# Optimization experiments

Measured on AMD Instinct MI355X. Metric: run time of the kernel, lower is better.

The kernel has to match this reference:

```python
import jax, jax.numpy as jnp
import numpy as np


def _l2norm(x, axis=1, eps=1e-12):
    n = jnp.sqrt(jnp.sum(x * x, axis=axis, keepdims=True))
    return x / jnp.maximum(n, eps)


def _update(query, keys, labels, class_counts, num_classes):
    # Vectorized form of Memory.update + get_update_query (train branch).
    m, d = keys.shape
    q = _l2norm(query, axis=1)                              # [N, d]
    score = q @ keys.T                                      # [N, m]
    s_q = jax.nn.softmax(score, axis=0)                     # softmax over queries
    s_m = jax.nn.softmax(score, axis=1)                     # softmax over memory slots
    gather = jnp.argmax(s_m, axis=1)                        # top-1 slot per query, [N]
    # per-slot scatter-reduce: sum_{i: argmax_i==j} s_q[i,j]/max_i s_q[i,j] * q[i]
    w = s_q / jnp.max(s_q, axis=0, keepdims=True)           # [N, m]
    onehot = (gather[:, None] == jnp.arange(m)[None, :]).astype(q.dtype)
    qu = (w * onehot).T @ q                                 # [m, d]
    part = m // num_classes
    slot_class = jnp.arange(m) // part                      # class id of each slot
    active = (slot_class[:, None] == labels[None, :]).any(axis=1)
    qu = jnp.where(active[:, None], qu, 0.0)                # only slots of present classes
    # count-weighted running-average update; torch loop overwrites
    # updated_keys_final each iteration, so only the LAST unique label
    # (torch.unique is sorted -> max) takes effect. Faithful to that.
    last = jnp.max(labels)
    count = jnp.sum(labels == last).astype(q.dtype)
    in_part = slot_class == last
    temp = jnp.where(in_part, class_counts[last], 1.0)[:, None]   # [m, 1]
    updated = temp * keys + qu
    temp2 = temp + jnp.where(in_part, count, 0.0)[:, None]
    return _l2norm(updated / temp2, axis=1)                 # [m, d]


def _read(embedding, mem, num_classes):
    # Memory.read: per-partition block_compare, score is detached in torch.
    m, d = mem.shape
    pr = m // (num_classes - 1)
    nblk = m // pr
    qr = embedding.reshape(d, -1).T                         # [Nq, d]
    blocks = mem.reshape(nblk, pr, d)

    def blk(b):
        s = jax.lax.stop_gradient(b @ qr.T)                 # [pr, Nq] (detached)
        return s.T @ b                                      # [Nq, d]

    return jax.vmap(blk)(blocks)                            # [nblk, Nq, d]


def setup_inputs():
    key = jax.random.key(0)
    k1, k2, k3, k4, k5 = jax.random.split(key, 5)
    N, d, m, C, Nq, L = 8192, 256, 4608, 9, 16384, 16
    return {
        "query": jax.random.normal(k1, (N, d), jnp.float32),
        "embeddings_src": jax.random.normal(k2, (d, Nq), jnp.float32),
        "embeddings_tgt": jax.random.normal(k3, (d, Nq), jnp.float32),
        "keys": _l2norm(jax.random.normal(k4, (m, d), jnp.float32), axis=1),
        "class_counts": jnp.ones((C,), jnp.float32),
        "labels": jax.random.randint(k5, (L,), 1, C).astype(jnp.int32),
        "num_classes": C,
    }


def reference(query, embeddings_src, embeddings_tgt, keys, class_counts, labels, num_classes):
    mem = _update(query, keys, labels, class_counts, num_classes)
    feat_src = _read(embeddings_src, mem, num_classes)
    feat_tgt = _read(embeddings_tgt, mem, num_classes)
    return jnp.stack([feat_src, feat_tgt])                  # [2, nblk, Nq, d]
```

## Files before the change

kernel.cpp:

```cpp
#include <hip/hip_runtime.h>
#include <math.h>

#define NQRY 8192
#define DIM  256
#define MS   4608
#define NQE  16384
#define NBLK 8
#define PRROWS 576

typedef __attribute__((ext_vector_type(8))) short bf16x8;
typedef __attribute__((ext_vector_type(4))) float f32x4;
typedef __attribute__((ext_vector_type(16))) float f32x16;


__device__ __forceinline__ unsigned ordf(float f) {
  unsigned u = __float_as_uint(f);
  return (u & 0x80000000u) ? ~u : (u | 0x80000000u);
}
__device__ __forceinline__ float unordf(unsigned u) {
  unsigned b = (u & 0x80000000u) ? (u & 0x7FFFFFFFu) : ~u;
  return __uint_as_float(b);
}
__device__ __forceinline__ unsigned short bf16rn(float x) {
  unsigned u = __float_as_uint(x);
  unsigned r = u + 0x7FFFu + ((u >> 16) & 1u);
  return (unsigned short)(r >> 16);
}
__device__ __forceinline__ void splitbf(float x, unsigned short& h, unsigned short& lo) {
  unsigned u = __float_as_uint(x);
  h = (unsigned short)(u >> 16);
  float hf = __uint_as_float(u & 0xFFFF0000u);
  lo = bf16rn(x - hf);
}

#define PREP_NBLK 18070
#define ZERO_N4   300160
__global__ __launch_bounds__(256) void k_prep(
    const float* __restrict__ query, float* __restrict__ q,
    unsigned short* __restrict__ qh, unsigned short* __restrict__ ql,
    const float* __restrict__ keys,
    unsigned short* __restrict__ kh, unsigned short* __restrict__ kl,
    const float* __restrict__ embS, const float* __restrict__ embT,
    unsigned short* __restrict__ ebT,
    float4* __restrict__ zp,
    const int* __restrict__ labels, const float* __restrict__ cc,
    float* __restrict__ sc) {
  __shared__ float tile[64][33];
  int b = blockIdx.x, t = threadIdx.x;
  if (b < 8192) {
    size_t idx = (size_t)b * DIM + t;
    float x = query[idx];
    float v = x * x;
    #pragma unroll
    for (int o = 32; o; o >>= 1) v += __shfl_down(v, o);
    float* s = &tile[0][0];
    if ((t & 63) == 0) s[t >> 6] = v;
    __syncthreads();
    float ss = (s[0] + s[1]) + (s[2] + s[3]);
    float qq = x / fmaxf(sqrtf(ss), 1e-12f);
    q[idx] = qq;
    unsigned short h, lo;
    splitbf(qq, h, lo);
    qh[idx] = h; ql[idx] = lo;
  } else if (b < 12800) {
    size_t idx = (size_t)(b - 8192) * 256 + t;
    unsigned short h, lo;
    splitbf(keys[idx], h, lo);
    kh[idx] = h; kl[idx] = lo;
  } else if (b < 16896) {
    int bb = b - 12800;
    int x = bb & 511, y = (bb >> 9) & 3, z = bb >> 11;
    const float* emb = z ? embT : embS;
    int n0 = x * 32, k0 = y * 64;
    int kl2 = t >> 5, nl = t & 31;
    #pragma unroll
    for (int i = 0; i < 8; i++)
      tile[kl2 * 8 + i][nl] = emb[(size_t)(k0 + kl2 * 8 + i) * NQE + n0 + nl];
    __syncthreads();
    int nl2 = t >> 3, kq = (t & 7) * 8;
    bf16x8 hv;
    #pragma unroll
    for (int j = 0; j < 8; j++) hv[j] = (short)bf16rn(tile[kq + j][nl2]);
    *(bf16x8*)(ebT + (size_t)z * NQE * DIM + (size_t)(n0 + nl2) * DIM + k0 + kq) = hv;
  } else if (b < 18069) {
    int i = (b - 16896) * 256 + t;
    if (i < ZERO_N4) zp[i] = float4{0.f, 0.f, 0.f, 0.f};
  } else {
    if (t < 64) {
      int l = (t < 16) ? labels[t] : (int)0x80000000;
      int mx = l;
      #pragma unroll
      for (int o = 32; o; o >>= 1) mx = max(mx, __shfl_down(mx, o));
      mx = __shfl(mx, 0);
      int cnt = (t < 16 && l == mx) ? 1 : 0;
      #pragma unroll
      for (int o = 32; o; o >>= 1) cnt += __shfl_down(cnt, o);
      unsigned amv = (t < 16) ? (1u << l) : 0u;
      #pragma unroll
      for (int o = 32; o; o >>= 1) amv |= __shfl_down(amv, o);
      if (t == 0) {
        sc[0] = __int_as_float(mx);
        sc[1] = (float)cnt;
        sc[2] = cc[mx];
        sc[3] = __uint_as_float(amv);
      }
    }
  }
}

__global__ __launch_bounds__(256) void k_scoremax(
    const unsigned short* __restrict__ qh, const unsigned short* __restrict__ ql,
    const unsigned short* __restrict__ kh, const unsigned short* __restrict__ kl,
    unsigned long long* __restrict__ rowbest, unsigned* __restrict__ colmax) {
  __shared__ __align__(16) char smem[32768];
  char* sA = smem;
  char* sB = smem + 16384;
  int tid = threadIdx.x;
  int n0 = blockIdx.x * 128, m0 = blockIdx.y * 128;
  int w = tid >> 6, lane = tid & 63;
  int wm = w >> 1, wn = w & 1;
  int l31 = lane & 31, hi5 = lane >> 5;
  int srow = tid >> 3, sc8 = tid & 7;
  f32x16 acc[2][2] = {};
  for (int kk = 0; kk < 8; kk++) {
    __syncthreads();
    #pragma unroll
    for (int t = 0; t < 8; t++) {
      int row = (t & 3) * 32 + srow;
      const unsigned short* hsrc = (t < 4) ? qh : kh;
      const unsigned short* lsrc = (t < 4) ? ql : kl;
      int base = (t < 4) ? m0 : n0;
      const unsigned short* src =
          ((sc8 < 4) ? hsrc : lsrc) + (size_t)(base + row) * DIM + kk * 32 + (sc8 & 3) * 8;
      char* dst = ((t < 4) ? sA : sB) + row * 128 + ((sc8 ^ (row & 7)) << 4);
      *(bf16x8*)dst = *(const bf16x8*)src;
    }
    __syncthreads();
    bf16x8 ah[2][2], al[2][2];
    #pragma unroll
    for (int fm = 0; fm < 2; fm++) {
      int ra = wm * 64 + fm * 32 + l31;
      #pragma unroll
      for (int h = 0; h < 2; h++) {
        int ch = h * 2 + hi5;
        ah[fm][h] = *(const bf16x8*)(sA + ra * 128 + ((ch ^ (ra & 7)) << 4));
        al[fm][h] = *(const bf16x8*)(sA + ra * 128 + (((ch + 4) ^ (ra & 7)) << 4));
      }
    }
    #pragma unroll
    for (int fn = 0; fn < 2; fn++) {
      int rb = wn * 64 + fn * 32 + l31;
      bf16x8 bh[2], bl[2];
      #pragma unroll
      for (int h = 0; h < 2; h++) {
        int ch = h * 2 + hi5;
        bh[h] = *(const bf16x8*)(sB + rb * 128 + ((ch ^ (rb & 7)) << 4));
        bl[h] = *(const bf16x8*)(sB + rb * 128 + (((ch + 4) ^ (rb & 7)) << 4));
      }
      #pragma unroll
      for (int fm = 0; fm < 2; fm++)
        #pragma unroll
        for (int h = 0; h < 2; h++) {
          acc[fm][fn] = __builtin_amdgcn_mfma_f32_32x32x16_bf16(ah[fm][h], bh[h], acc[fm][fn], 0, 0, 0);
          acc[fm][fn] = __builtin_amdgcn_mfma_f32_32x32x16_bf16(ah[fm][h], bl[h], acc[fm][fn], 0, 0, 0);
          acc[fm][fn] = __builtin_amdgcn_mfma_f32_32x32x16_bf16(al[fm][h], bh[h], acc[fm][fn], 0, 0, 0);
        }
    }
  }
  #pragma unroll
  for (int fm = 0; fm < 2; fm++) {
    #pragma unroll
    for (int reg = 0; reg < 16; reg++) {
      unsigned long long p = 0ull;
      #pragma unroll
      for (int fn = 0; fn < 2; fn++) {
        float v = acc[fm][fn][reg];
        unsigned ng = (unsigned)(n0 + wn * 64 + fn * 32 + l31);
        unsigned long long cand =
            ((unsigned long long)ordf(v) << 32) | (unsigned long long)(0xFFFFFFFFu - ng);
        if (cand > p) p = cand;
      }
      #pragma unroll
      for (int o = 1; o < 32; o <<= 1) {
        unsigned long long t2 = __shfl_xor(p, o);
        if (t2 > p) p = t2;
      }
      if (l31 == 0) {
        int rl = (reg & 3) + 8 * (reg >> 2) + 4 * hi5;
        atomicMax(rowbest + (m0 + wm * 64 + fm * 32 + rl), p);
      }
    }
  }
  #pragma unroll
  for (int fn = 0; fn < 2; fn++) {
    float v = -3.4e38f;
    #pragma unroll
    for (int fm = 0; fm < 2; fm++)
      #pragma unroll
      for (int reg = 0; reg < 16; reg++) v = fmaxf(v, acc[fm][fn][reg]);
    v = fmaxf(v, __shfl_xor(v, 32));
    if (hi5 == 0) atomicMax(colmax + (n0 + wn * 64 + fn * 32 + l31), ordf(v));
  }
}

__global__ __launch_bounds__(256) void k_rowscatter(
    const unsigned long long* __restrict__ rowbest, const unsigned* __restrict__ colmax,
    const float* __restrict__ q, float* __restrict__ qu) {
  int i = blockIdx.x, t = threadIdx.x;
  unsigned long long p = rowbest[i];
  int g = (int)(0xFFFFFFFFu - (unsigned)(p & 0xFFFFFFFFull));
  float sv = unordf((unsigned)(p >> 32));
  float w = expf(sv - unordf(colmax[g]));
  atomicAdd(qu + (size_t)g * DIM + t, w * q[(size_t)i * DIM + t]);
}

__global__ __launch_bounds__(256) void k_mem(const float* __restrict__ keys,
                                             const float* __restrict__ qu,
                                             const float* __restrict__ sc,
                                             float* __restrict__ memr) {
  int j = blockIdx.x, t = threadIdx.x;
  int last = __float_as_int(sc[0]);
  float count = sc[1], ccl = sc[2];
  unsigned am = __float_as_uint(sc[3]);
  int cls = j >> 9;
  bool inp = (cls == last);
  float temp = inp ? ccl : 1.0f;
  float quv = ((am >> cls) & 1u) ? qu[(size_t)j * DIM + t] : 0.0f;
  float u = temp * keys[(size_t)j * DIM + t] + quv;
  float temp2 = temp + (inp ? count : 0.0f);
  float v = u / temp2;
  float vv = v * v;
  #pragma unroll
  for (int o = 32; o; o >>= 1) vv += __shfl_down(vv, o);
  __shared__ float s[4];
  if ((t & 63) == 0) s[t >> 6] = vv;
  __syncthreads();
  float ss = (s[0] + s[1]) + (s[2] + s[3]);
  memr[(size_t)j * DIM + t] = v / fmaxf(sqrtf(ss), 1e-12f);
}

__global__ __launch_bounds__(256) void k_gram(const float* __restrict__ memr,
                                              unsigned short* __restrict__ Gb) {
  __shared__ float As[16][64];
  __shared__ float Bs[16][64];
  int b = blockIdx.z;
  int kxc = blockIdx.x * 64;
  int kyr = blockIdx.y * 64;
  const float* Ab = memr + (size_t)b * PRROWS * DIM;
  int tid = threadIdx.x, tx = tid & 15, ty = tid >> 4;
  int lp = tid >> 4;
  int lk = (tid & 15) * 4;
  float acc[4][4] = {};
  for (int p0 = 0; p0 < PRROWS; p0 += 16) {
    float4 av = *(const float4*)(Ab + (size_t)(p0 + lp) * DIM + kyr + lk);
    float4 bv = *(const float4*)(Ab + (size_t)(p0 + lp) * DIM + kxc + lk);
    __syncthreads();
    *(float4*)&As[lp][lk] = av;
    *(float4*)&Bs[lp][lk] = bv;
    __syncthreads();
    #pragma unroll
    for (int p = 0; p < 16; p++) {
      float a[4], c[4];
      *(float4*)&a[0] = *(const float4*)&As[p][ty * 4];
      *(float4*)&c[0] = *(const float4*)&Bs[p][tx * 4];
      #pragma unroll
      for (int r = 0; r < 4; r++)
        #pragma unroll
        for (int s2 = 0; s2 < 4; s2++)
          acc[r][s2] = fmaf(a[r], c[s2], acc[r][s2]);
    }
  }
  #pragma unroll
  for (int r = 0; r < 4; r++)
    #pragma unroll
    for (int s2 = 0; s2 < 4; s2++)
      Gb[(size_t)b * DIM * DIM + (size_t)(kyr + ty * 4 + r) * DIM + kxc + tx * 4 + s2] =
          bf16rn(acc[r][s2]);
}

__global__ __launch_bounds__(256) void k_read_mfma(
    const unsigned short* __restrict__ ebT, const unsigned short* __restrict__ Gb,
    float* __restrict__ out) {
  __shared__ __align__(16) char smem[32768];
  char* sA = smem;
  char* sB = smem + 16384;
  int tid = threadIdx.x;
  int eb = blockIdx.z;
  const unsigned short* ea = ebT + (size_t)(eb >> 3) * NQE * DIM;
  const unsigned short* gb = Gb + (size_t)(eb & 7) * DIM * DIM;
  int n0 = blockIdx.x * 128, d0 = blockIdx.y * 128;
  int w = tid >> 6, l = tid & 63;
  int wm = w >> 1, wn = w & 1;
  int lr = l >> 4, lc = l & 15;
  f32x4 acc[4][4] = {};
  for (int kk = 0; kk < 4; kk++) {
    __syncthreads();
    #pragma unroll
    for (int t = 0; t < 4; t++) {
      int c = t * 256 + tid;
      int row = c >> 3, cc = c & 7;
      int ldsb = row * 128 + ((cc * 16) ^ ((row & 7) << 4));
      size_t gA = (size_t)(n0 + row) * DIM + kk * 64 + cc * 8;
      size_t gB = (size_t)(d0 + row) * DIM + kk * 64 + cc * 8;
      *(bf16x8*)(sA + ldsb) = *(const bf16x8*)(ea + gA);
      *(bf16x8*)(sB + ldsb) = *(const bf16x8*)(gb + gB);
    }
    __syncthreads();
    #pragma unroll
    for (int st = 0; st < 2; st++) {
      bf16x8 af[4], bf[4];
      #pragma unroll
      for (int f = 0; f < 4; f++) {
        int ra = wm * 64 + f * 16 + lc;
        int ka = (st * 64 + lr * 16) ^ ((ra & 7) << 4);
        af[f] = *(const bf16x8*)(sA + ra * 128 + ka);
        int rb = wn * 64 + f * 16 + lc;
        int kb = (st * 64 + lr * 16) ^ ((rb & 7) << 4);
        bf[f] = *(const bf16x8*)(sB + rb * 128 + kb);
      }
      #pragma unroll
      for (int fm = 0; fm < 4; fm++)
        #pragma unroll
        for (int fn = 0; fn < 4; fn++)
          acc[fm][fn] = __builtin_amdgcn_mfma_f32_16x16x32_bf16(af[fm], bf[fn], acc[fm][fn], 0, 0, 0);
    }
  }
  size_t base = (size_t)eb * NQE * DIM;
  #pragma unroll
  for (int fm = 0; fm < 4; fm++)
    #pragma unroll
    for (int rg = 0; rg < 4; rg++) {
      int n = n0 + wm * 64 + fm * 16 + lr * 4 + rg;
      float* op = out + base + (size_t)n * DIM + d0 + wn * 64 + lc;
      #pragma unroll
      for (int fn = 0; fn < 4; fn++) op[fn * 16] = acc[fm][fn][rg];
    }
}

extern "C" void kernel_launch(void* const* d_in, const int* in_sizes, int n_in,
                              void* d_out, int out_size, void* d_ws, size_t ws_size,
                              hipStream_t stream) {
  const float* query  = (const float*)d_in[0];
  const float* embS   = (const float*)d_in[1];
  const float* embT   = (const float*)d_in[2];
  const float* keys   = (const float*)d_in[3];
  const float* cc     = (const float*)d_in[4];
  const int*   labels = (const int*)d_in[5];
  float* out = (float*)d_out;

  float* q                     = out;
  unsigned short* qh           = (unsigned short*)(out + 2097152);
  unsigned short* ql           = (unsigned short*)(out + 3145728);
  unsigned short* kh           = (unsigned short*)(out + 4194304);
  unsigned short* kl           = (unsigned short*)(out + 4784128);
  float* qu                    = out + 5373952;
  unsigned long long* rowbest  = (unsigned long long*)(out + 6553600);
  unsigned* colmax             = (unsigned*)(out + 6569984);
  float* memr                  = out + 6574592;

  unsigned short* ebT = (unsigned short*)d_ws;
  unsigned short* Gb  = (unsigned short*)((char*)d_ws + 16777216);
  float* sc           = (float*)((char*)d_ws + 17825792);

  k_prep<<<PREP_NBLK, 256, 0, stream>>>(query, q, qh, ql, keys, kh, kl,
                                        embS, embT, ebT, (float4*)qu,
                                        labels, cc, sc);
  k_scoremax<<<dim3(MS / 128, NQRY / 128), 256, 0, stream>>>(qh, ql, kh, kl, rowbest, colmax);
  k_rowscatter<<<NQRY, 256, 0, stream>>>(rowbest, colmax, q, qu);
  k_mem<<<MS, 256, 0, stream>>>(keys, qu, sc, memr);
  k_gram<<<dim3(4, 4, NBLK), 256, 0, stream>>>(memr, Gb);
  k_read_mfma<<<dim3(NQE / 128, DIM / 128, 2 * NBLK), 256, 0, stream>>>(ebT, Gb, out);
}
```

Baseline: 235.1 us.

## Prefetch next K-slice into registers and switch scoremax to 16x16x32 MFMA

The score/argmax kernel now loads the next K-slice of the query and key bf16 hi/lo tiles into registers while the MFMAs for the current slice run, so global load latency overlaps compute. It also swaps the 32x32x16 MFMA tiling for 16x16x32 fragments (4x4 accumulators per wave) and adjusts the row/column max reductions and atomics to the new lane layout. The prefetch costs extra registers per thread, which may lower occupancy, and the smaller MFMA tiles change LDS read patterns and reduction shuffle counts.

```diff
diff --git a/kernel.cpp b/kernel.cpp
--- a/kernel.cpp
+++ b/kernel.cpp
@@ -10,7 +10,6 @@
 
 typedef __attribute__((ext_vector_type(8))) short bf16x8;
 typedef __attribute__((ext_vector_type(4))) float f32x4;
-typedef __attribute__((ext_vector_type(16))) float f32x16;
 
 
 __device__ __forceinline__ unsigned ordf(float f) {
@@ -119,87 +118,98 @@
   int n0 = blockIdx.x * 128, m0 = blockIdx.y * 128;
   int w = tid >> 6, lane = tid & 63;
   int wm = w >> 1, wn = w & 1;
-  int l31 = lane & 31, hi5 = lane >> 5;
+  int lr = lane >> 4, lc = lane & 15;
   int srow = tid >> 3, sc8 = tid & 7;
-  f32x16 acc[2][2] = {};
+  bf16x8 pf[8];
+  #pragma unroll
+  for (int t = 0; t < 8; t++) {
+    int row = (t & 3) * 32 + srow;
+    const unsigned short* hsrc = (t < 4) ? qh : kh;
+    const unsigned short* lsrc = (t < 4) ? ql : kl;
+    int base = (t < 4) ? m0 : n0;
+    pf[t] = *(const bf16x8*)(((sc8 < 4) ? hsrc : lsrc) +
+                             (size_t)(base + row) * DIM + (sc8 & 3) * 8);
+  }
+  f32x4 acc[4][4] = {};
   for (int kk = 0; kk < 8; kk++) {
     __syncthreads();
     #pragma unroll
     for (int t = 0; t < 8; t++) {
       int row = (t & 3) * 32 + srow;
-      const unsigned short* hsrc = (t < 4) ? qh : kh;
-      const unsigned short* lsrc = (t < 4) ? ql : kl;
-      int base = (t < 4) ? m0 : n0;
-      const unsigned short* src =
-          ((sc8 < 4) ? hsrc : lsrc) + (size_t)(base + row) * DIM + kk * 32 + (sc8 & 3) * 8;
       char* dst = ((t < 4) ? sA : sB) + row * 128 + ((sc8 ^ (row & 7)) << 4);
-      *(bf16x8*)dst = *(const bf16x8*)src;
-    }
-    __syncthreads();
-    bf16x8 ah[2][2], al[2][2];
-    #pragma unroll
-    for (int fm = 0; fm < 2; fm++) {
-      int ra = wm * 64 + fm * 32 + l31;
-      #pragma unroll
-      for (int h = 0; h < 2; h++) {
-        int ch = h * 2 + hi5;
-        ah[fm][h] = *(const bf16x8*)(sA + ra * 128 + ((ch ^ (ra & 7)) << 4));
-        al[fm][h] = *(const bf16x8*)(sA + ra * 128 + (((ch + 4) ^ (ra & 7)) << 4));
-      }
-    }
-    #pragma unroll
-    for (int fn = 0; fn < 2; fn++) {
-      int rb = wn * 64 + fn * 32 + l31;
+      *(bf16x8*)dst = pf[t];
+    }
+    __syncthreads();
+    if (kk < 7) {
+      #pragma unroll
+      for (int t = 0; t < 8; t++) {
+        int row = (t & 3) * 32 + srow;
+        const unsigned short* hsrc = (t < 4) ? qh : kh;
+        const unsigned short* lsrc = (t < 4) ? ql : kl;
+        int base = (t < 4) ? m0 : n0;
+        pf[t] = *(const bf16x8*)(((sc8 < 4) ? hsrc : lsrc) +
+                                 (size_t)(base + row) * DIM + (kk + 1) * 32 + (sc8 & 3) * 8);
+      }
+    }
+    bf16x8 ah[4], al[4];
+    #pragma unroll
+    for (int f = 0; f < 4; f++) {
+      int ra = wm * 64 + f * 16 + lc;
+      ah[f] = *(const bf16x8*)(sA + ra * 128 + ((lr ^ (ra & 7)) << 4));
+      al[f] = *(const bf16x8*)(sA + ra * 128 + (((lr + 4) ^ (ra & 7)) << 4));
+    }
+    #pragma unroll
+    for (int half = 0; half < 2; half++) {
       bf16x8 bh[2], bl[2];
       #pragma unroll
-      for (int h = 0; h < 2; h++) {
-        int ch = h * 2 + hi5;
-        bh[h] = *(const bf16x8*)(sB + rb * 128 + ((ch ^ (rb & 7)) << 4));
-        bl[h] = *(const bf16x8*)(sB + rb * 128 + (((ch + 4) ^ (rb & 7)) << 4));
-      }
-      #pragma unroll
-      for (int fm = 0; fm < 2; fm++)
+      for (int f2 = 0; f2 < 2; f2++) {
+        int rb = wn * 64 + (half * 2 + f2) * 16 + lc;
+        bh[f2] = *(const bf16x8*)(sB + rb * 128 + ((lr ^ (rb & 7)) << 4));
+        bl[f2] = *(const bf16x8*)(sB + rb * 128 + (((lr + 4) ^ (rb & 7)) << 4));
+      }
+      #pragma unroll
+      for (int fm = 0; fm < 4; fm++)
         #pragma unroll
-        for (int h = 0; h < 2; h++) {
-          acc[fm][fn] = __builtin_amdgcn_mfma_f32_32x32x16_bf16(ah[fm][h], bh[h], acc[fm][fn], 0, 0, 0);
-          acc[fm][fn] = __builtin_amdgcn_mfma_f32_32x32x16_bf16(ah[fm][h], bl[h], acc[fm][fn], 0, 0, 0);
-          acc[fm][fn] = __builtin_amdgcn_mfma_f32_32x32x16_bf16(al[fm][h], bh[h], acc[fm][fn], 0, 0, 0);
+        for (int f2 = 0; f2 < 2; f2++) {
+          int fn = half * 2 + f2;
+          acc[fm][fn] = __builtin_amdgcn_mfma_f32_16x16x32_bf16(ah[fm], bh[f2], acc[fm][fn], 0, 0, 0);
+          acc[fm][fn] = __builtin_amdgcn_mfma_f32_16x16x32_bf16(ah[fm], bl[f2], acc[fm][fn], 0, 0, 0);
+          acc[fm][fn] = __builtin_amdgcn_mfma_f32_16x16x32_bf16(al[fm], bh[f2], acc[fm][fn], 0, 0, 0);
         }
     }
   }
   #pragma unroll
-  for (int fm = 0; fm < 2; fm++) {
-    #pragma unroll
-    for (int reg = 0; reg < 16; reg++) {
+  for (int fm = 0; fm < 4; fm++) {
+    #pragma unroll
+    for (int rg = 0; rg < 4; rg++) {
       unsigned long long p = 0ull;
       #pragma unroll
-      for (int fn = 0; fn < 2; fn++) {
-        float v = acc[fm][fn][reg];
-        unsigned ng = (unsigned)(n0 + wn * 64 + fn * 32 + l31);
+      for (int fn = 0; fn < 4; fn++) {
+        float v = acc[fm][fn][rg];
+        unsigned ng = (unsigned)(n0 + wn * 64 + fn * 16 + lc);
         unsigned long long cand =
             ((unsigned long long)ordf(v) << 32) | (unsigned long long)(0xFFFFFFFFu - ng);
         if (cand > p) p = cand;
       }
       #pragma unroll
-      for (int o = 1; o < 32; o <<= 1) {
+      for (int o = 1; o < 16; o <<= 1) {
         unsigned long long t2 = __shfl_xor(p, o);
         if (t2 > p) p = t2;
       }
-      if (l31 == 0) {
-        int rl = (reg & 3) + 8 * (reg >> 2) + 4 * hi5;
-        atomicMax(rowbest + (m0 + wm * 64 + fm * 32 + rl), p);
-      }
-    }
-  }
-  #pragma unroll
-  for (int fn = 0; fn < 2; fn++) {
+      if (lc == 0)
+        atomicMax(rowbest + (m0 + wm * 64 + fm * 16 + lr * 4 + rg), p);
+    }
+  }
+  #pragma unroll
+  for (int fn = 0; fn < 4; fn++) {
     float v = -3.4e38f;
     #pragma unroll
-    for (int fm = 0; fm < 2; fm++)
-      #pragma unroll
-      for (int reg = 0; reg < 16; reg++) v = fmaxf(v, acc[fm][fn][reg]);
+    for (int fm = 0; fm < 4; fm++)
+      #pragma unroll
+      for (int rg = 0; rg < 4; rg++) v = fmaxf(v, acc[fm][fn][rg]);
+    v = fmaxf(v, __shfl_xor(v, 16));
     v = fmaxf(v, __shfl_xor(v, 32));
-    if (hi5 == 0) atomicMax(colmax + (n0 + wn * 64 + fn * 32 + l31), ordf(v));
+    if (lr == 0) atomicMax(colmax + (n0 + wn * 64 + fn * 16 + lc), ordf(v));
   }
 }
 
```

Result: faster. 214.4 us (-8.8%).
